# Kernel optimization log

Hardware: AMD Instinct MI355X
Metric: run time of the kernel (lower is better)

Reference implementation:

```python
import jax, jax.numpy as jnp
import numpy as np

D = 256      # model dim
H = 8        # heads
DH = 32      # dim per head
M = 110      # nb random features = int(32*ln(32))
DEPTH = 6
DFF = 1024   # ff_mult * D


def _layer_norm(x, g, b):
    mu = jnp.mean(x, -1, keepdims=True)
    var = jnp.mean(jnp.square(x - mu), -1, keepdims=True)
    return (x - mu) * jax.lax.rsqrt(var + 1e-5) * g + b


def _softmax_kernel(x, proj, is_query):
    # FAVOR+ positive softmax kernel features (performer-pytorch softmax_kernel)
    dn = x.shape[-1] ** -0.25
    ratio = proj.shape[0] ** -0.5
    xd = jnp.einsum('bhnd,md->bhnm', x * dn, proj)
    diag = 0.5 * jnp.sum(jnp.square(x), -1, keepdims=True) * dn * dn
    stab = jnp.max(xd, -1, keepdims=True) if is_query else jnp.max(xd)
    return ratio * (jnp.exp(xd - diag - stab) + 1e-3)


def _linear_attention(q, k, v):
    # non-causal linear attention: O(N*m*d) instead of O(N^2)
    k_sum = jnp.sum(k, axis=2)                               # [B,H,m]
    d_inv = 1.0 / jnp.einsum('bhnm,bhm->bhn', q, k_sum)      # [B,H,N]
    ctx = jnp.einsum('bhnm,bhnd->bhmd', k, v)                # [B,H,m,dh]
    return jnp.einsum('bhnm,bhmd,bhn->bhnd', q, ctx, d_inv)


def _forward(expr, token_emb, cls_token, ln1_g, ln1_b, Wq, bq, Wk, bk, Wv, bv,
             Wo, bo, ln2_g, ln2_b, W1, b1, W2, b2, proj_mat, Wp, bp, top_k_genes):
    B = expr.shape[0]
    vals, _ = jax.lax.top_k(expr, top_k_genes)               # [B, k] sorted desc (matches torch.topk)
    # preprocess: L1 normalize (eps=1e-12 like F.normalize) -> *1e4 -> log1p -> 7 bins
    norm = vals / jnp.maximum(jnp.sum(jnp.abs(vals), -1, keepdims=True), 1e-12)
    e = jnp.log1p(norm * 10000.0)
    bins = jnp.linspace(0.0, jnp.max(e), 8)
    # torch.bucketize(right=False) == searchsorted side='left'
    tokens = jnp.clip(jnp.searchsorted(bins[:-1], e, side='left'), 0, 6)
    x = jnp.concatenate([jnp.broadcast_to(cls_token, (B, 1, D)), token_emb[tokens]], axis=1)
    N = x.shape[1]
    for i in range(DEPTH):
        # pre-norm FAVOR+ attention block
        h = _layer_norm(x, ln1_g[i], ln1_b[i])
        q = (h @ Wq[i] + bq[i]).reshape(B, N, H, DH).transpose(0, 2, 1, 3)
        k = (h @ Wk[i] + bk[i]).reshape(B, N, H, DH).transpose(0, 2, 1, 3)
        v = (h @ Wv[i] + bv[i]).reshape(B, N, H, DH).transpose(0, 2, 1, 3)
        qp = _softmax_kernel(q, proj_mat[i], True)
        kp = _softmax_kernel(k, proj_mat[i], False)
        o = _linear_attention(qp, kp, v).transpose(0, 2, 1, 3).reshape(B, N, D)
        x = x + o @ Wo[i] + bo[i]
        # pre-norm FFN block (GELU exact, like torch default)
        h2 = _layer_norm(x, ln2_g[i], ln2_b[i])
        x = x + jax.nn.gelu(h2 @ W1[i] + b1[i], approximate=False) @ W2[i] + b2[i]
    return x[:, 0] @ Wp + bp


def setup_inputs() -> dict:
    key = jax.random.key(0)
    ks = jax.random.split(key, 12)
    s = 0.02
    return {
        'expr': jax.random.uniform(ks[0], (8, 16906), dtype=jnp.float32),
        'token_emb': jax.random.normal(ks[1], (7, D), dtype=jnp.float32) * s,
        'cls_token': jax.random.normal(ks[2], (1, 1, D), dtype=jnp.float32),
        'ln1_g': jnp.ones((DEPTH, D), jnp.float32),
        'ln1_b': jnp.zeros((DEPTH, D), jnp.float32),
        'Wq': jax.random.normal(ks[3], (DEPTH, D, D), dtype=jnp.float32) * s,
        'bq': jnp.zeros((DEPTH, D), jnp.float32),
        'Wk': jax.random.normal(ks[4], (DEPTH, D, D), dtype=jnp.float32) * s,
        'bk': jnp.zeros((DEPTH, D), jnp.float32),
        'Wv': jax.random.normal(ks[5], (DEPTH, D, D), dtype=jnp.float32) * s,
        'bv': jnp.zeros((DEPTH, D), jnp.float32),
        'Wo': jax.random.normal(ks[6], (DEPTH, D, D), dtype=jnp.float32) * s,
        'bo': jnp.zeros((DEPTH, D), jnp.float32),
        'ln2_g': jnp.ones((DEPTH, D), jnp.float32),
        'ln2_b': jnp.zeros((DEPTH, D), jnp.float32),
        'W1': jax.random.normal(ks[7], (DEPTH, D, DFF), dtype=jnp.float32) * s,
        'b1': jnp.zeros((DEPTH, DFF), jnp.float32),
        'W2': jax.random.normal(ks[8], (DEPTH, DFF, D), dtype=jnp.float32) * s,
        'b2': jnp.zeros((DEPTH, D), jnp.float32),
        'proj_mat': jax.random.normal(ks[9], (DEPTH, M, DH), dtype=jnp.float32),
        'Wp': jax.random.normal(ks[10], (D, D), dtype=jnp.float32) * s,
        'bp': jnp.zeros((D,), jnp.float32),
        'top_k_genes': 2048,
    }


def reference(expr, token_emb, cls_token, ln1_g, ln1_b, Wq, bq, Wk, bk, Wv, bv,
              Wo, bo, ln2_g, ln2_b, W1, b1, W2, b2, proj_mat, Wp, bp, top_k_genes):
    return _forward(expr, token_emb, cls_token, ln1_g, ln1_b, Wq, bq, Wk, bk, Wv, bv,
                    Wo, bo, ln2_g, ln2_b, W1, b1, W2, b2, proj_mat, Wp, bp, top_k_genes)
```

## Files before the change

kernel.cpp:

```cpp
#include <hip/hip_runtime.h>
#include <hip/hip_bf16.h>

#define B_    8
#define NG    16906
#define KSEL  2048
#define D_    256
#define H_    8
#define DH    32
#define M_    110
#define DEPTH_ 6
#define DFF_  1024
#define N_    2049
#define BN_   (B_*N_)
#define QS    768
#define NC    8
#define NTILES 33
#define CTXE  (M_*33)
#define CTXN2 (64*CTXE)
#define NIT_TK 17

static constexpr float DN    = 0.42044820762685725f;
static constexpr float DN2   = 0.17677669529663687f;
static constexpr float RATIO = 0.09534625892455922f;

typedef __attribute__((ext_vector_type(8))) short s8v;
typedef __attribute__((ext_vector_type(4))) float f4v;

__device__ __forceinline__ unsigned floatToOrdered(float f){
  unsigned b = __float_as_uint(f);
  return (b & 0x80000000u) ? ~b : (b | 0x80000000u);
}
__device__ __forceinline__ float orderedToFloat(unsigned u){
  unsigned b = (u & 0x80000000u) ? (u & 0x7FFFFFFFu) : ~u;
  return __uint_as_float(b);
}
__device__ __forceinline__ unsigned short f2us(float f){
  __hip_bfloat16 b = __float2bfloat16(f);
  return *reinterpret_cast<unsigned short*>(&b);
}

__global__ __launch_bounds__(1024) void topk_k(const float* __restrict__ expr,
                                               float* __restrict__ selected)
{
  __shared__ unsigned hist[256];
  __shared__ unsigned sPrefix;
  __shared__ int sKK;
  __shared__ unsigned cGT, cEQ;
  int b = blockIdx.x, tid = threadIdx.x;
  const float* row = expr + (long)b*NG;
  unsigned rb[NIT_TK];
  #pragma unroll
  for (int i = 0; i < NIT_TK; i++){
    int idx = tid + i*1024;
    rb[i] = (idx < NG) ? __float_as_uint(row[idx]) : 0u;
  }
  if (tid == 0){ sPrefix = 0u; sKK = KSEL; }
  __syncthreads();
  for (int pass = 0; pass < 4; ++pass){
    int shift = 24 - pass*8;
    if (tid < 256) hist[tid] = 0u;
    __syncthreads();
    unsigned pref = sPrefix;
    #pragma unroll
    for (int i = 0; i < NIT_TK; i++){
      int idx = tid + i*1024;
      unsigned bits = rb[i];
      bool ok = (idx < NG) && ((pass == 0) || ((bits >> (shift + 8)) == pref));
      if (ok) atomicAdd(&hist[(bits >> shift) & 255u], 1u);
    }
    __syncthreads();
    if (tid == 0){
      int kk = sKK; unsigned cum = 0; int sel = 0;
      for (int j = 255; j >= 0; --j){
        unsigned c = hist[j];
        if (cum + c >= (unsigned)kk){ sel = j; break; }
        cum += c;
      }
      sPrefix = (pref << 8) | (unsigned)sel;
      sKK = kk - (int)cum;
    }
    __syncthreads();
  }
  unsigned T = sPrefix; int needEQ = sKK; int base = KSEL - needEQ;
  if (tid == 0){ cGT = 0u; cEQ = 0u; }
  __syncthreads();
  #pragma unroll
  for (int i = 0; i < NIT_TK; i++){
    int idx = tid + i*1024;
    if (idx < NG){
      unsigned bits = rb[i];
      if (bits > T){
        unsigned p = atomicAdd(&cGT, 1u);
        selected[(long)b*KSEL + p] = __uint_as_float(bits);
      } else if (bits == T){
        unsigned p = atomicAdd(&cEQ, 1u);
        if ((int)p < needEQ) selected[(long)b*KSEL + base + p] = __uint_as_float(bits);
      }
    }
  }
}

__global__ __launch_bounds__(256) void nsum_k(const float* __restrict__ selected,
                                              float* __restrict__ bsum, float* __restrict__ bv0)
{
  __shared__ float rs[256], rm[256];
  int b = blockIdx.x, tid = threadIdx.x;
  float s = 0.f, m = -INFINITY;
  for (int i = tid; i < KSEL; i += 256){ float v = selected[(long)b*KSEL + i]; s += v; m = fmaxf(m, v); }
  rs[tid] = s; rm[tid] = m; __syncthreads();
  for (int k = 128; k > 0; k >>= 1){
    if (tid < k){ rs[tid] += rs[tid + k]; rm[tid] = fmaxf(rm[tid], rm[tid + k]); }
    __syncthreads();
  }
  if (tid == 0){ bsum[b] = rs[0]; bv0[b] = rm[0]; }
}

__global__ __launch_bounds__(64) void emax_k(const float* __restrict__ bsum,
                                             const float* __restrict__ bv0,
                                             float* __restrict__ emaxp)
{
  int tid = threadIdx.x;
  float e = -INFINITY;
  if (tid < B_) e = log1pf(bv0[tid] / fmaxf(bsum[tid], 1e-12f) * 10000.0f);
  #pragma unroll
  for (int m = 1; m < 64; m <<= 1) e = fmaxf(e, __shfl_xor(e, m));
  if (tid == 0) emaxp[0] = e;
}

__global__ __launch_bounds__(64) void embed_k(const float* __restrict__ selected,
    const float* __restrict__ bsum, const float* __restrict__ emaxp,
    const float* __restrict__ temb, const float* __restrict__ cls,
    float* __restrict__ x)
{
  int rowi = blockIdx.x;
  int b = rowi / N_, n = rowi % N_;
  int tid = threadIdx.x;
  const float* src;
  if (n == 0){
    src = cls;
  } else {
    float val = selected[(long)b*KSEL + (n - 1)];
    float e = log1pf(val / fmaxf(bsum[b], 1e-12f) * 10000.0f);
    float step = emaxp[0] / 7.0f;
    int cnt = 0;
    #pragma unroll
    for (int i = 0; i < 7; i++) cnt += (((float)i * step) < e) ? 1 : 0;
    int tok = cnt > 6 ? 6 : cnt;
    src = temb + (long)tok * D_;
  }
  float4 o = *(const float4*)(src + tid*4);
  *(float4*)(x + (long)rowi*D_ + tid*4) = o;
}

__global__ __launch_bounds__(256) void ln_k(const float* __restrict__ x,
    unsigned short* __restrict__ out,
    const float* __restrict__ g, const float* __restrict__ bb)
{
  int row = blockIdx.x*4 + (threadIdx.x >> 6);
  int lane = threadIdx.x & 63;
  float4 v = *(const float4*)(x + (long)row*D_ + lane*4);
  float s = v.x + v.y + v.z + v.w;
  float q = v.x*v.x + v.y*v.y + v.z*v.z + v.w*v.w;
  #pragma unroll
  for (int m = 1; m < 64; m <<= 1){ s += __shfl_xor(s, m); q += __shfl_xor(q, m); }
  float mu  = s * (1.0f/D_);
  float var = q * (1.0f/D_) - mu*mu;
  float inv = 1.0f / sqrtf(fmaxf(var, 0.f) + 1e-5f);
  float4 gu = *(const float4*)(g + lane*4);
  float4 bu = *(const float4*)(bb + lane*4);
  ushort4 o;
  o.x = f2us((v.x - mu)*inv*gu.x + bu.x);
  o.y = f2us((v.y - mu)*inv*gu.y + bu.y);
  o.z = f2us((v.z - mu)*inv*gu.z + bu.z);
  o.w = f2us((v.w - mu)*inv*gu.w + bu.w);
  *(ushort4*)(out + (long)row*D_ + lane*4) = o;
}

__global__ __launch_bounds__(256) void wcvt_k(const float* __restrict__ src, long srcL,
    unsigned short* __restrict__ dst, long dstL, int K, int N)
{
  __shared__ float t[32][33];
  int n0 = blockIdx.x*32, k0 = blockIdx.y*32, L = blockIdx.z;
  int tx = threadIdx.x & 31, ty = threadIdx.x >> 5;
  const float* s = src + (long)L*srcL;
  for (int i = ty; i < 32; i += 8)
    t[i][tx] = s[(long)(k0+i)*N + n0 + tx];
  __syncthreads();
  unsigned short* d = dst + (long)L*dstL;
  for (int i = ty; i < 32; i += 8)
    d[(long)(n0 + i)*K + k0 + tx] = f2us(t[tx][i]);
}

__global__ __launch_bounds__(256) void pcvt_k(const float* __restrict__ proj,
                                              unsigned short* __restrict__ projb,
                                              unsigned* __restrict__ kmaxb)
{
  int L = blockIdx.x;
  if (blockIdx.x == 0 && threadIdx.x < DEPTH_) kmaxb[threadIdx.x] = 0u;
  for (int i = threadIdx.x; i < 112*32; i += 256){
    int m = i >> 5, d = i & 31;
    float v = (m < M_) ? proj[(long)L*M_*DH + m*DH + d] : 0.f;
    projb[(long)L*112*32 + i] = f2us(v);
  }
}

__global__ __launch_bounds__(256) void bcat_k(const float* __restrict__ bq,
    const float* __restrict__ bk, const float* __restrict__ bv,
    float* __restrict__ bqkv)
{
  int L = blockIdx.x;
  for (int i = threadIdx.x; i < QS; i += 256){
    float v = (i < 256) ? bq[L*256 + i] : (i < 512) ? bk[L*256 + i - 256] : bv[L*256 + i - 512];
    bqkv[(long)L*QS + i] = v;
  }
}

template<int ACT, int RES, int OUTBF>
__global__ __launch_bounds__(256) void bgemm_k(
    const unsigned short* __restrict__ A, long lda,
    const unsigned short* __restrict__ Bt,
    const float* __restrict__ bias,
    const float* __restrict__ res,
    float* __restrict__ Cf, unsigned short* __restrict__ Cb,
    int M, int Nn, int K)
{
  __shared__ __attribute__((aligned(16))) unsigned short As[128*40];
  __shared__ __attribute__((aligned(16))) unsigned short Bs[128*40];
  int tid = threadIdx.x;
  int rowBlk = blockIdx.x*128, colBlk = blockIdx.y*128;
  int w = tid >> 6, lane = tid & 63;
  int wrow = (w >> 1)*64, wcol = (w & 1)*64;
  int fr = lane & 15, fk = (lane >> 4)*8, fq = lane >> 4;
  int srh = tid >> 2, sk8 = (tid & 3)*8;

  f4v acc[4][4];
  #pragma unroll
  for (int r = 0; r < 4; r++)
    #pragma unroll
    for (int c = 0; c < 4; c++) acc[r][c] = (f4v){0.f, 0.f, 0.f, 0.f};

  s8v pa[2], pb[2];
  #pragma unroll
  for (int half = 0; half < 2; half++){
    int r = half*64 + srh;
    int ar = rowBlk + r;
    pa[half] = (ar < M) ? *(const s8v*)(A + (long)ar*lda + sk8) : (s8v){0,0,0,0,0,0,0,0};
    pb[half] = *(const s8v*)(Bt + (long)(colBlk + r)*K + sk8);
  }

  for (int kt = 0; kt < K; kt += 32){
    __syncthreads();
    #pragma unroll
    for (int half = 0; half < 2; half++){
      int r = half*64 + srh;
      *(s8v*)&As[r*40 + sk8] = pa[half];
      *(s8v*)&Bs[r*40 + sk8] = pb[half];
    }
    __syncthreads();
    if (kt + 32 < K){
      int kn = kt + 32;
      #pragma unroll
      for (int half = 0; half < 2; half++){
        int r = half*64 + srh;
        int ar = rowBlk + r;
        pa[half] = (ar < M) ? *(const s8v*)(A + (long)ar*lda + kn + sk8) : (s8v){0,0,0,0,0,0,0,0};
        pb[half] = *(const s8v*)(Bt + (long)(colBlk + r)*K + kn + sk8);
      }
    }
    s8v a[4], b[4];
    #pragma unroll
    for (int r = 0; r < 4; r++) a[r] = *(s8v*)&As[(wrow + r*16 + fr)*40 + fk];
    #pragma unroll
    for (int c = 0; c < 4; c++) b[c] = *(s8v*)&Bs[(wcol + c*16 + fr)*40 + fk];
    #pragma unroll
    for (int r = 0; r < 4; r++)
      #pragma unroll
      for (int c = 0; c < 4; c++)
        acc[r][c] = __builtin_amdgcn_mfma_f32_16x16x32_bf16(a[r], b[c], acc[r][c], 0, 0, 0);
  }

  #pragma unroll
  for (int c = 0; c < 4; c++){
    int col = colBlk + wcol + c*16 + fr;
    float bz = bias[col];
    #pragma unroll
    for (int r = 0; r < 4; r++){
      #pragma unroll
      for (int j = 0; j < 4; j++){
        int row = rowBlk + wrow + r*16 + fq*4 + j;
        if (row < M){
          float val = acc[r][c][j] + bz;
          if (ACT == 1) val = 0.5f * val * (1.0f + erff(val * 0.70710678118654752f));
          if (RES) val += res[(long)row*Nn + col];
          if (OUTBF) Cb[(long)row*Nn + col] = f2us(val);
          else       Cf[(long)row*Nn + col] = val;
        }
      }
    }
  }
}

__global__ __launch_bounds__(256) void gemm_k(
    const float* __restrict__ A, long lda,
    const float* __restrict__ Bw, long ldb,
    const float* __restrict__ bias,
    float* __restrict__ Cf,
    int M, int Nn, int K)
{
  __shared__ float As[16][64];
  __shared__ float Bs[16][64];
  int tid = threadIdx.x;
  int tx = tid & 15, ty = tid >> 4;
  int rowBlk = blockIdx.x * 64, colBlk = blockIdx.y * 64;
  int am = tid >> 2, ak = (tid & 3) * 4;
  int bk = tid >> 4, bc = (tid & 15) * 4;
  float acc[4][4];
  #pragma unroll
  for (int i = 0; i < 4; i++)
    #pragma unroll
    for (int j = 0; j < 4; j++) acc[i][j] = 0.f;

  for (int kt = 0; kt < K; kt += 16){
    float4 av = make_float4(0.f, 0.f, 0.f, 0.f);
    int ar = rowBlk + am;
    if (ar < M) av = *(const float4*)(A + (long)ar*lda + kt + ak);
    As[ak+0][am] = av.x; As[ak+1][am] = av.y; As[ak+2][am] = av.z; As[ak+3][am] = av.w;
    float4 bv4 = *(const float4*)(Bw + (long)(kt + bk)*ldb + colBlk + bc);
    Bs[bk][bc+0] = bv4.x; Bs[bk][bc+1] = bv4.y;
    Bs[bk][bc+2] = bv4.z; Bs[bk][bc+3] = bv4.w;
    __syncthreads();
    #pragma unroll
    for (int kk = 0; kk < 16; kk++){
      float4 a4 = *(const float4*)&As[kk][ty*4];
      float4 b4 = *(const float4*)&Bs[kk][tx*4];
      acc[0][0] += a4.x*b4.x; acc[0][1] += a4.x*b4.y; acc[0][2] += a4.x*b4.z; acc[0][3] += a4.x*b4.w;
      acc[1][0] += a4.y*b4.x; acc[1][1] += a4.y*b4.y; acc[1][2] += a4.y*b4.z; acc[1][3] += a4.y*b4.w;
      acc[2][0] += a4.z*b4.x; acc[2][1] += a4.z*b4.y; acc[2][2] += a4.z*b4.z; acc[2][3] += a4.z*b4.w;
      acc[3][0] += a4.w*b4.x; acc[3][1] += a4.w*b4.y; acc[3][2] += a4.w*b4.z; acc[3][3] += a4.w*b4.w;
    }
    __syncthreads();
  }
  int r0 = rowBlk + ty*4, c0 = colBlk + tx*4;
  float bz[4];
  #pragma unroll
  for (int j = 0; j < 4; j++) bz[j] = bias[c0 + j];
  #pragma unroll
  for (int i = 0; i < 4; i++){
    int r = r0 + i;
    if (r < M){
      #pragma unroll
      for (int j = 0; j < 4; j++)
        Cf[(long)r*Nn + c0 + j] = acc[i][j] + bz[j];
    }
  }
}

__global__ __launch_bounds__(256) void kmax2_k(const float* __restrict__ qkv,
    const unsigned short* __restrict__ projb, unsigned* __restrict__ kmaxb)
{
  __shared__ __attribute__((aligned(16))) unsigned short ks[64*40];
  __shared__ float red[4];
  int t = blockIdx.x, h = blockIdx.y, b = blockIdx.z;
  int tid = threadIdx.x, w = tid >> 6, lane = tid & 63;
  int fr = lane & 15, fq = lane >> 4, fk = fq*8;
  int n0 = t*64;
  #pragma unroll
  for (int it = 0; it < 2; it++){
    int tok = it*32 + (tid >> 3), d4 = tid & 7;
    int n = n0 + tok;
    bool vld = (n < N_);
    long gb = ((long)(b*N_ + (vld ? n : 0)))*QS + 256 + h*DH + d4*4;
    float4 kv = vld ? *(const float4*)(qkv + gb) : make_float4(0,0,0,0);
    ushort4 ku; ku.x=f2us(kv.x); ku.y=f2us(kv.y); ku.z=f2us(kv.z); ku.w=f2us(kv.w);
    *(ushort4*)&ks[tok*40 + d4*4] = ku;
  }
  __syncthreads();
  s8v bk_ = *(s8v*)&ks[(w*16 + fr)*40 + fk];
  float mx = -INFINITY;
  int n_ = w*16 + fr;
  bool nv = (n0 + n_ < N_);
  #pragma unroll
  for (int mt = 0; mt < 7; mt++){
    s8v ap = *(const s8v*)(projb + (mt*16 + fr)*32 + fk);
    f4v z = (f4v){0.f,0.f,0.f,0.f};
    f4v xd = __builtin_amdgcn_mfma_f32_16x16x32_bf16(ap, bk_, z, 0, 0, 0);
    #pragma unroll
    for (int j = 0; j < 4; j++){
      int m = mt*16 + fq*4 + j;
      float v = (nv && m < M_) ? xd[j]*DN : -INFINITY;
      mx = fmaxf(mx, v);
    }
  }
  #pragma unroll
  for (int mk = 1; mk < 64; mk <<= 1) mx = fmaxf(mx, __shfl_xor(mx, mk));
  if (lane == 0) red[w] = mx;
  __syncthreads();
  if (tid == 0){
    float g = fmaxf(fmaxf(red[0], red[1]), fmaxf(red[2], red[3]));
    atomicMax(kmaxb, floatToOrdered(g));
  }
}

__global__ __launch_bounds__(256) void fctx_k(const float* __restrict__ qkv,
    const unsigned short* __restrict__ projb,
    const unsigned* __restrict__ kmaxb, float* __restrict__ partials)
{
  __shared__ __attribute__((aligned(16))) unsigned short ks[64*40];
  __shared__ __attribute__((aligned(16))) unsigned short vt[48*72];
  __shared__ __attribute__((aligned(16))) unsigned short kps[112*72];
  __shared__ float diags[64];
  int c = blockIdx.x, h = blockIdx.y, b = blockIdx.z;
  int tid = threadIdx.x, w = tid >> 6, lane = tid & 63;
  int fr = lane & 15, fq = lane >> 4, fk = fq*8;
  float kmax = orderedToFloat(kmaxb[0]);

  for (int i = tid; i < 15*72; i += 256) vt[33*72 + i] = 0;
  if (tid < 64) vt[32*72 + tid] = f2us(1.0f);

  s8v ap[7];
  #pragma unroll
  for (int mt = 0; mt < 7; mt++)
    ap[mt] = *(const s8v*)(projb + (mt*16 + fr)*32 + fk);

  int mt0 = w, mt1 = w + 4;
  f4v acc0[3], acc1[3];
  #pragma unroll
  for (int dt = 0; dt < 3; dt++){ acc0[dt] = (f4v){0.f,0.f,0.f,0.f}; acc1[dt] = (f4v){0.f,0.f,0.f,0.f}; }

  for (int t = c; t < NTILES; t += NC){
    int n0 = t*64;
    __syncthreads();
    #pragma unroll
    for (int it = 0; it < 2; it++){
      int tok = it*32 + (tid >> 3), d4 = tid & 7;
      int n = n0 + tok;
      bool vld = (n < N_);
      long gb = ((long)(b*N_ + (vld ? n : 0)))*QS + 256 + h*DH + d4*4;
      float4 kv = vld ? *(const float4*)(qkv + gb) : make_float4(0,0,0,0);
      float4 vv = vld ? *(const float4*)(qkv + gb + 256) : make_float4(0,0,0,0);
      ushort4 ku; ku.x=f2us(kv.x); ku.y=f2us(kv.y); ku.z=f2us(kv.z); ku.w=f2us(kv.w);
      *(ushort4*)&ks[tok*40 + d4*4] = ku;
      vt[(d4*4+0)*72 + tok] = f2us(vv.x);
      vt[(d4*4+1)*72 + tok] = f2us(vv.y);
      vt[(d4*4+2)*72 + tok] = f2us(vv.z);
      vt[(d4*4+3)*72 + tok] = f2us(vv.w);
      float sq = kv.x*kv.x + kv.y*kv.y + kv.z*kv.z + kv.w*kv.w;
      sq += __shfl_xor(sq, 1); sq += __shfl_xor(sq, 2); sq += __shfl_xor(sq, 4);
      if (d4 == 0) diags[tok] = 0.5f * DN2 * sq;
    }
    __syncthreads();
    s8v bk_ = *(s8v*)&ks[(w*16 + fr)*40 + fk];
    int n_ = w*16 + fr;
    bool nv = (n0 + n_ < N_);
    float dgn = diags[n_];
    #pragma unroll
    for (int mt = 0; mt < 7; mt++){
      f4v z = (f4v){0.f,0.f,0.f,0.f};
      f4v xd = __builtin_amdgcn_mfma_f32_16x16x32_bf16(ap[mt], bk_, z, 0, 0, 0);
      #pragma unroll
      for (int j = 0; j < 4; j++){
        float kp = nv ? RATIO*(expf(xd[j]*DN - dgn - kmax) + 1e-3f) : 0.f;
        kps[(mt*16 + fq*4 + j)*72 + n_] = f2us(kp);
      }
    }
    __syncthreads();
    #pragma unroll
    for (int kst = 0; kst < 2; kst++){
      int ko = kst*32 + fk;
      s8v b0 = *(s8v*)&vt[( 0 + fr)*72 + ko];
      s8v b1 = *(s8v*)&vt[(16 + fr)*72 + ko];
      s8v b2 = *(s8v*)&vt[(32 + fr)*72 + ko];
      s8v a0 = *(s8v*)&kps[(mt0*16 + fr)*72 + ko];
      acc0[0] = __builtin_amdgcn_mfma_f32_16x16x32_bf16(a0, b0, acc0[0], 0, 0, 0);
      acc0[1] = __builtin_amdgcn_mfma_f32_16x16x32_bf16(a0, b1, acc0[1], 0, 0, 0);
      acc0[2] = __builtin_amdgcn_mfma_f32_16x16x32_bf16(a0, b2, acc0[2], 0, 0, 0);
      if (mt1 < 7){
        s8v a1 = *(s8v*)&kps[(mt1*16 + fr)*72 + ko];
        acc1[0] = __builtin_amdgcn_mfma_f32_16x16x32_bf16(a1, b0, acc1[0], 0, 0, 0);
        acc1[1] = __builtin_amdgcn_mfma_f32_16x16x32_bf16(a1, b1, acc1[1], 0, 0, 0);
        acc1[2] = __builtin_amdgcn_mfma_f32_16x16x32_bf16(a1, b2, acc1[2], 0, 0, 0);
      }
    }
  }
  long pb = ((long)c*64 + (b*H_ + h))*CTXE;
  #pragma unroll
  for (int dt = 0; dt < 3; dt++){
    int d = dt*16 + fr;
    if (d < 33){
      #pragma unroll
      for (int j = 0; j < 4; j++){
        int m0 = mt0*16 + fq*4 + j;
        if (m0 < M_) partials[pb + m0*33 + d] = acc0[dt][j];
        if (mt1 < 7){
          int m1 = mt1*16 + fq*4 + j;
          if (m1 < M_) partials[pb + m1*33 + d] = acc1[dt][j];
        }
      }
    }
  }
}

__global__ __launch_bounds__(256) void ctxred2_k(const float* __restrict__ partials,
                                                 float* __restrict__ ctxf)
{
  int i = blockIdx.x*256 + threadIdx.x;
  if (i >= CTXN2) return;
  float s = 0.f;
  #pragma unroll
  for (int c = 0; c < NC; c++) s += partials[(long)c*CTXN2 + i];
  ctxf[i] = s;
}

__global__ __launch_bounds__(256) void attn3_k(const float* __restrict__ qkv,
    const float* __restrict__ ctxf, const unsigned short* __restrict__ projb,
    unsigned short* __restrict__ ob)
{
  __shared__ __attribute__((aligned(16))) unsigned short qs[64*40];
  __shared__ __attribute__((aligned(16))) unsigned short qps[64*136];
  __shared__ __attribute__((aligned(16))) unsigned short cst[48*136];
  __shared__ float diags[64];
  __shared__ float dens[64];
  int t = blockIdx.x, h = blockIdx.y, b = blockIdx.z;
  int tid = threadIdx.x, w = tid >> 6, lane = tid & 63;
  int fr = lane & 15, fq = lane >> 4, fk = fq*8;
  int n0 = t*64;
  long cbase = ((long)(b*H_ + h))*CTXE;

  for (int i = tid; i < 64*16; i += 256)
    qps[(i >> 4)*136 + 112 + (i & 15)] = 0;

  #pragma unroll
  for (int it = 0; it < 2; it++){
    int tok = it*32 + (tid >> 3), d4 = tid & 7;
    int n = n0 + tok;
    bool vld = (n < N_);
    long gb = ((long)(b*N_ + (vld ? n : 0)))*QS + h*DH + d4*4;
    float4 qv = vld ? *(const float4*)(qkv + gb) : make_float4(0,0,0,0);
    ushort4 qu; qu.x=f2us(qv.x); qu.y=f2us(qv.y); qu.z=f2us(qv.z); qu.w=f2us(qv.w);
    *(ushort4*)&qs[tok*40 + d4*4] = qu;
    float sq = qv.x*qv.x + qv.y*qv.y + qv.z*qv.z + qv.w*qv.w;
    sq += __shfl_xor(sq, 1); sq += __shfl_xor(sq, 2); sq += __shfl_xor(sq, 4);
    if (d4 == 0) diags[tok] = 0.5f * DN2 * sq;
  }
  for (int i = tid; i < 48*128; i += 256){
    int d = i >> 7, m = i & 127;
    float v = (d < 33 && m < M_) ? ctxf[cbase + (long)m*33 + d] : 0.f;
    cst[d*136 + m] = f2us(v);
  }
  __syncthreads();

  s8v bq_ = *(s8v*)&qs[(w*16 + fr)*40 + fk];
  int n_ = w*16 + fr;
  bool nv = (n0 + n_ < N_);
  float dgn = diags[n_];
  f4v xdv[7];
  #pragma unroll
  for (int mt = 0; mt < 7; mt++){
    s8v ap = *(const s8v*)(projb + (mt*16 + fr)*32 + fk);
    f4v z = (f4v){0.f,0.f,0.f,0.f};
    xdv[mt] = __builtin_amdgcn_mfma_f32_16x16x32_bf16(ap, bq_, z, 0, 0, 0);
  }
  float mx = -INFINITY;
  #pragma unroll
  for (int mt = 0; mt < 7; mt++)
    #pragma unroll
    for (int j = 0; j < 4; j++){
      int m = mt*16 + fq*4 + j;
      if (m < M_) mx = fmaxf(mx, xdv[mt][j]*DN);
    }
  mx = fmaxf(mx, __shfl_xor(mx, 16));
  mx = fmaxf(mx, __shfl_xor(mx, 32));
  #pragma unroll
  for (int mt = 0; mt < 7; mt++)
    #pragma unroll
    for (int j = 0; j < 4; j++){
      int m = mt*16 + fq*4 + j;
      float qp = (nv && m < M_) ? RATIO*(expf(xdv[mt][j]*DN - dgn - mx) + 1e-3f) : 0.f;
      qps[n_*136 + m] = f2us(qp);
    }
  __syncthreads();

  f4v acc[3];
  acc[0] = (f4v){0,0,0,0}; acc[1] = (f4v){0,0,0,0}; acc[2] = (f4v){0,0,0,0};
  #pragma unroll
  for (int ks = 0; ks < 4; ks++){
    int ko = ks*32 + fk;
    s8v bqp = *(s8v*)&qps[(w*16 + fr)*136 + ko];
    #pragma unroll
    for (int dt = 0; dt < 3; dt++){
      s8v ac = *(s8v*)&cst[(dt*16 + fr)*136 + ko];
      acc[dt] = __builtin_amdgcn_mfma_f32_16x16x32_bf16(ac, bqp, acc[dt], 0, 0, 0);
    }
  }
  if (fq == 0) dens[n_] = acc[2][0];
  __syncthreads();
  float dinv = 1.0f / dens[n_];
  if (nv){
    long obase = ((long)(b*N_ + n0 + n_))*D_ + h*DH;
    #pragma unroll
    for (int dt = 0; dt < 2; dt++){
      ushort4 wv;
      wv.x = f2us(acc[dt][0]*dinv);
      wv.y = f2us(acc[dt][1]*dinv);
      wv.z = f2us(acc[dt][2]*dinv);
      wv.w = f2us(acc[dt][3]*dinv);
      *(ushort4*)(ob + obase + dt*16 + fq*4) = wv;
    }
  }
}

extern "C" void kernel_launch(void* const* d_in, const int* in_sizes, int n_in,
                              void* d_out, int out_size, void* d_ws, size_t ws_size,
                              hipStream_t stream)
{
  const float* expr = (const float*)d_in[0];
  const float* temb = (const float*)d_in[1];
  const float* cls  = (const float*)d_in[2];
  const float* ln1g = (const float*)d_in[3];
  const float* ln1b = (const float*)d_in[4];
  const float* Wq   = (const float*)d_in[5];
  const float* bq   = (const float*)d_in[6];
  const float* Wk   = (const float*)d_in[7];
  const float* bk   = (const float*)d_in[8];
  const float* Wv   = (const float*)d_in[9];
  const float* bv   = (const float*)d_in[10];
  const float* Wo   = (const float*)d_in[11];
  const float* bo   = (const float*)d_in[12];
  const float* ln2g = (const float*)d_in[13];
  const float* ln2b = (const float*)d_in[14];
  const float* W1   = (const float*)d_in[15];
  const float* b1   = (const float*)d_in[16];
  const float* W2   = (const float*)d_in[17];
  const float* b2   = (const float*)d_in[18];
  const float* proj = (const float*)d_in[19];
  const float* Wp   = (const float*)d_in[20];
  const float* bp   = (const float*)d_in[21];
  (void)in_sizes; (void)n_in; (void)out_size; (void)ws_size;

  char* w = (char*)d_ws;
  size_t off = 0;
  auto alloc = [&](size_t bytes) -> char* {
    char* p = w + off;
    off = (off + bytes + 255) & ~(size_t)255;
    return p;
  };
  float*    selected = (float*)alloc((size_t)B_*KSEL*4);
  float*    bsum     = (float*)alloc(B_*4);
  float*    bv0      = (float*)alloc(B_*4);
  float*    emaxp    = (float*)alloc(4);
  unsigned* kmaxb    = (unsigned*)alloc(DEPTH_*4);
  float*    ctxf     = (float*)alloc((size_t)CTXN2*4);
  float*          x  = (float*)alloc((size_t)BN_*D_*4);
  unsigned short* h  = (unsigned short*)alloc((size_t)BN_*D_*2);
  float*        qkv  = (float*)alloc((size_t)BN_*QS*4);
  unsigned short* Wqkvt = (unsigned short*)alloc((size_t)DEPTH_*QS*D_*2);
  unsigned short* Wot = (unsigned short*)alloc((size_t)DEPTH_*D_*D_*2);
  unsigned short* W1t = (unsigned short*)alloc((size_t)DEPTH_*D_*DFF_*2);
  unsigned short* W2t = (unsigned short*)alloc((size_t)DEPTH_*DFF_*D_*2);
  unsigned short* projb = (unsigned short*)alloc((size_t)DEPTH_*112*32*2);
  float*    bqkv     = (float*)alloc((size_t)DEPTH_*QS*4);
  unsigned short* ffi = (unsigned short*)qkv;
  float*     partials = (float*)h;

  wcvt_k<<<dim3(8, 8, DEPTH_),  256, 0, stream>>>(Wq, (long)D_*D_, Wqkvt + 0,      (long)QS*D_, D_, D_);
  wcvt_k<<<dim3(8, 8, DEPTH_),  256, 0, stream>>>(Wk, (long)D_*D_, Wqkvt + 256*D_, (long)QS*D_, D_, D_);
  wcvt_k<<<dim3(8, 8, DEPTH_),  256, 0, stream>>>(Wv, (long)D_*D_, Wqkvt + 512*D_, (long)QS*D_, D_, D_);
  wcvt_k<<<dim3(8, 8, DEPTH_),  256, 0, stream>>>(Wo, (long)D_*D_,   Wot, (long)D_*D_,   D_, D_);
  wcvt_k<<<dim3(32, 8, DEPTH_), 256, 0, stream>>>(W1, (long)D_*DFF_, W1t, (long)D_*DFF_, D_, DFF_);
  wcvt_k<<<dim3(8, 32, DEPTH_), 256, 0, stream>>>(W2, (long)DFF_*D_, W2t, (long)DFF_*D_, DFF_, D_);
  pcvt_k<<<DEPTH_, 256, 0, stream>>>(proj, projb, kmaxb);
  bcat_k<<<DEPTH_, 256, 0, stream>>>(bq, bk, bv, bqkv);

  topk_k<<<B_, 1024, 0, stream>>>(expr, selected);
  nsum_k<<<B_, 256, 0, stream>>>(selected, bsum, bv0);
  emax_k<<<1, 64, 0, stream>>>(bsum, bv0, emaxp);
  embed_k<<<BN_, 64, 0, stream>>>(selected, bsum, emaxp, temb, cls, x);

  for (int L = 0; L < DEPTH_; L++){
    const unsigned short* pjb = projb + (size_t)L*112*32;
    ln_k<<<BN_/4, 256, 0, stream>>>(x, h, ln1g + L*D_, ln1b + L*D_);
    bgemm_k<0,0,0><<<dim3(129,6), 256, 0, stream>>>(h, D_, Wqkvt + (size_t)L*QS*D_, bqkv + (size_t)L*QS, nullptr, qkv, nullptr, BN_, QS, D_);
    kmax2_k<<<dim3(NTILES, H_, B_), 256, 0, stream>>>(qkv, pjb, kmaxb + L);
    fctx_k<<<dim3(NC, H_, B_), 256, 0, stream>>>(qkv, pjb, kmaxb + L, partials);
    ctxred2_k<<<(CTXN2 + 255)/256, 256, 0, stream>>>(partials, ctxf);
    attn3_k<<<dim3(NTILES, H_, B_), 256, 0, stream>>>(qkv, ctxf, pjb, h);
    bgemm_k<0,1,0><<<dim3(129,2), 256, 0, stream>>>(h, D_, Wot + (size_t)L*D_*D_, bo + L*D_, x, x, nullptr, BN_, D_, D_);
    ln_k<<<BN_/4, 256, 0, stream>>>(x, h, ln2g + L*D_, ln2b + L*D_);
    bgemm_k<1,0,1><<<dim3(129,8), 256, 0, stream>>>(h, D_, W1t + (size_t)L*D_*DFF_, b1 + L*DFF_, nullptr, nullptr, ffi, BN_, DFF_, D_);
    bgemm_k<0,1,0><<<dim3(129,2), 256, 0, stream>>>(ffi, DFF_, W2t + (size_t)L*DFF_*D_, b2 + L*D_, x, x, nullptr, BN_, D_, DFF_);
  }
  gemm_k<<<dim3(1,4), 256, 0, stream>>>(x, (long)N_*D_, Wp, D_, bp,
                                        (float*)d_out, B_, D_, D_);
}
```

Before: 1.539 ms.

## Privatize topk histograms, aggregate atomics, stage bf16 GEMM output, swap grid order

The top-k radix select now uses one histogram per wavefront to reduce atomic contention, and it does the final scatter with wave-level ballot aggregation instead of per-thread atomics. The bf16-output GEMM epilogue (the FFN up-projection with GELU) writes its tile to shared memory first and then stores it with coalesced 16-byte writes. GEMM grids are transposed so that column blocks vary fastest, meant to improve reuse of A rows across consecutive blocks. The staging buffer enlarges shared memory for the OUTBF variant, which may reduce occupancy.

Measured after the change: 1.426 ms. 1.08x faster.

```diff
diff --git a/kernel.cpp b/kernel.cpp
--- a/kernel.cpp
+++ b/kernel.cpp
@@ -42,11 +42,12 @@
 __global__ __launch_bounds__(1024) void topk_k(const float* __restrict__ expr,
                                                float* __restrict__ selected)
 {
-  __shared__ unsigned hist[256];
+  __shared__ unsigned histw[16*256];
   __shared__ unsigned sPrefix;
   __shared__ int sKK;
   __shared__ unsigned cGT, cEQ;
   int b = blockIdx.x, tid = threadIdx.x;
+  int wv = tid >> 6, lane = tid & 63;
   const float* row = expr + (long)b*NG;
   unsigned rb[NIT_TK];
   #pragma unroll
@@ -55,10 +56,9 @@
     rb[i] = (idx < NG) ? __float_as_uint(row[idx]) : 0u;
   }
   if (tid == 0){ sPrefix = 0u; sKK = KSEL; }
-  __syncthreads();
   for (int pass = 0; pass < 4; ++pass){
     int shift = 24 - pass*8;
-    if (tid < 256) hist[tid] = 0u;
+    for (int i = tid; i < 16*256; i += 1024) histw[i] = 0u;
     __syncthreads();
     unsigned pref = sPrefix;
     #pragma unroll
@@ -66,13 +66,20 @@
       int idx = tid + i*1024;
       unsigned bits = rb[i];
       bool ok = (idx < NG) && ((pass == 0) || ((bits >> (shift + 8)) == pref));
-      if (ok) atomicAdd(&hist[(bits >> shift) & 255u], 1u);
+      if (ok) atomicAdd(&histw[wv*256 + ((bits >> shift) & 255u)], 1u);
+    }
+    __syncthreads();
+    if (tid < 256){
+      unsigned s = 0;
+      #pragma unroll
+      for (int w = 0; w < 16; w++) s += histw[w*256 + tid];
+      histw[tid] = s;
     }
     __syncthreads();
     if (tid == 0){
       int kk = sKK; unsigned cum = 0; int sel = 0;
       for (int j = 255; j >= 0; --j){
-        unsigned c = hist[j];
+        unsigned c = histw[j];
         if (cum + c >= (unsigned)kk){ sel = j; break; }
         cum += c;
       }
@@ -87,14 +94,30 @@
   #pragma unroll
   for (int i = 0; i < NIT_TK; i++){
     int idx = tid + i*1024;
-    if (idx < NG){
-      unsigned bits = rb[i];
-      if (bits > T){
-        unsigned p = atomicAdd(&cGT, 1u);
-        selected[(long)b*KSEL + p] = __uint_as_float(bits);
-      } else if (bits == T){
-        unsigned p = atomicAdd(&cEQ, 1u);
-        if ((int)p < needEQ) selected[(long)b*KSEL + base + p] = __uint_as_float(bits);
+    bool v = (idx < NG);
+    unsigned bits = rb[i];
+    bool gt = v && (bits > T);
+    unsigned long long mgt = __ballot(gt);
+    if (mgt){
+      int leader = __ffsll((long long)mgt) - 1;
+      unsigned wbase = 0;
+      if (lane == leader) wbase = atomicAdd(&cGT, (unsigned)__popcll(mgt));
+      wbase = __shfl(wbase, leader);
+      if (gt){
+        int pre = __popcll(mgt & ((1ULL << lane) - 1ULL));
+        selected[(long)b*KSEL + wbase + pre] = __uint_as_float(bits);
+      }
+    }
+    bool eq = v && (bits == T);
+    unsigned long long meq = __ballot(eq);
+    if (meq){
+      int leader = __ffsll((long long)meq) - 1;
+      unsigned wbase = 0;
+      if (lane == leader) wbase = atomicAdd(&cEQ, (unsigned)__popcll(meq));
+      wbase = __shfl(wbase, leader);
+      if (eq){
+        int pos = (int)wbase + __popcll(meq & ((1ULL << lane) - 1ULL));
+        if (pos < needEQ) selected[(long)b*KSEL + base + pos] = __uint_as_float(bits);
       }
     }
   }
@@ -224,10 +247,11 @@
     float* __restrict__ Cf, unsigned short* __restrict__ Cb,
     int M, int Nn, int K)
 {
-  __shared__ __attribute__((aligned(16))) unsigned short As[128*40];
-  __shared__ __attribute__((aligned(16))) unsigned short Bs[128*40];
+  __shared__ __attribute__((aligned(16))) unsigned short smem[OUTBF ? 128*132 : 2*128*40];
+  unsigned short* As = smem;
+  unsigned short* Bs = smem + 128*40;
   int tid = threadIdx.x;
-  int rowBlk = blockIdx.x*128, colBlk = blockIdx.y*128;
+  int colBlk = blockIdx.x*128, rowBlk = blockIdx.y*128;
   int w = tid >> 6, lane = tid & 63;
   int wrow = (w >> 1)*64, wcol = (w & 1)*64;
   int fr = lane & 15, fk = (lane >> 4)*8, fq = lane >> 4;
@@ -279,21 +303,47 @@
         acc[r][c] = __builtin_amdgcn_mfma_f32_16x16x32_bf16(a[r], b[c], acc[r][c], 0, 0, 0);
   }
 
-  #pragma unroll
-  for (int c = 0; c < 4; c++){
-    int col = colBlk + wcol + c*16 + fr;
-    float bz = bias[col];
-    #pragma unroll
-    for (int r = 0; r < 4; r++){
+  if (OUTBF){
+    __syncthreads();
+    unsigned short* Cs = smem;
+    #pragma unroll
+    for (int c = 0; c < 4; c++){
+      int col = wcol + c*16 + fr;
+      float bz = bias[colBlk + col];
       #pragma unroll
-      for (int j = 0; j < 4; j++){
-        int row = rowBlk + wrow + r*16 + fq*4 + j;
-        if (row < M){
+      for (int r = 0; r < 4; r++){
+        #pragma unroll
+        for (int j = 0; j < 4; j++){
+          int rrow = wrow + r*16 + fq*4 + j;
           float val = acc[r][c][j] + bz;
           if (ACT == 1) val = 0.5f * val * (1.0f + erff(val * 0.70710678118654752f));
-          if (RES) val += res[(long)row*Nn + col];
-          if (OUTBF) Cb[(long)row*Nn + col] = f2us(val);
-          else       Cf[(long)row*Nn + col] = val;
+          Cs[rrow*132 + col] = f2us(val);
+        }
+      }
+    }
+    __syncthreads();
+    for (int ci = tid; ci < 128*16; ci += 256){
+      int rrow = ci >> 4, ch = ci & 15;
+      int grow = rowBlk + rrow;
+      if (grow < M)
+        *(s8v*)(Cb + (long)grow*Nn + colBlk + ch*8) = *(s8v*)&Cs[rrow*132 + ch*8];
+    }
+  } else {
+    #pragma unroll
+    for (int c = 0; c < 4; c++){
+      int col = colBlk + wcol + c*16 + fr;
+      float bz = bias[col];
+      #pragma unroll
+      for (int r = 0; r < 4; r++){
+        #pragma unroll
+        for (int j = 0; j < 4; j++){
+          int row = rowBlk + wrow + r*16 + fq*4 + j;
+          if (row < M){
+            float val = acc[r][c][j] + bz;
+            if (ACT == 1) val = 0.5f * val * (1.0f + erff(val * 0.70710678118654752f));
+            if (RES) val += res[(long)row*Nn + col];
+            Cf[(long)row*Nn + col] = val;
+          }
         }
       }
     }
@@ -679,15 +729,15 @@
   for (int L = 0; L < DEPTH_; L++){
     const unsigned short* pjb = projb + (size_t)L*112*32;
     ln_k<<<BN_/4, 256, 0, stream>>>(x, h, ln1g + L*D_, ln1b + L*D_);
-    bgemm_k<0,0,0><<<dim3(129,6), 256, 0, stream>>>(h, D_, Wqkvt + (size_t)L*QS*D_, bqkv + (size_t)L*QS, nullptr, qkv, nullptr, BN_, QS, D_);
+    bgemm_k<0,0,0><<<dim3(6,129), 256, 0, stream>>>(h, D_, Wqkvt + (size_t)L*QS*D_, bqkv + (size_t)L*QS, nullptr, qkv, nullptr, BN_, QS, D_);
     kmax2_k<<<dim3(NTILES, H_, B_), 256, 0, stream>>>(qkv, pjb, kmaxb + L);
     fctx_k<<<dim3(NC, H_, B_), 256, 0, stream>>>(qkv, pjb, kmaxb + L, partials);
     ctxred2_k<<<(CTXN2 + 255)/256, 256, 0, stream>>>(partials, ctxf);
     attn3_k<<<dim3(NTILES, H_, B_), 256, 0, stream>>>(qkv, ctxf, pjb, h);
-    bgemm_k<0,1,0><<<dim3(129,2), 256, 0, stream>>>(h, D_, Wot + (size_t)L*D_*D_, bo + L*D_, x, x, nullptr, BN_, D_, D_);
+    bgemm_k<0,1,0><<<dim3(2,129), 256, 0, stream>>>(h, D_, Wot + (size_t)L*D_*D_, bo + L*D_, x, x, nullptr, BN_, D_, D_);
     ln_k<<<BN_/4, 256, 0, stream>>>(x, h, ln2g + L*D_, ln2b + L*D_);
-    bgemm_k<1,0,1><<<dim3(129,8), 256, 0, stream>>>(h, D_, W1t + (size_t)L*D_*DFF_, b1 + L*DFF_, nullptr, nullptr, ffi, BN_, DFF_, D_);
-    bgemm_k<0,1,0><<<dim3(129,2), 256, 0, stream>>>(ffi, DFF_, W2t + (size_t)L*DFF_*D_, b2 + L*D_, x, x, nullptr, BN_, D_, DFF_);
+    bgemm_k<1,0,1><<<dim3(8,129), 256, 0, stream>>>(h, D_, W1t + (size_t)L*D_*DFF_, b1 + L*DFF_, nullptr, nullptr, ffi, BN_, DFF_, D_);
+    bgemm_k<0,1,0><<<dim3(2,129), 256, 0, stream>>>(ffi, DFF_, W2t + (size_t)L*DFF_*D_, b2 + L*D_, x, x, nullptr, BN_, D_, DFF_);
   }
   gemm_k<<<dim3(1,4), 256, 0, stream>>>(x, (long)N_*D_, Wp, D_, bp,
                                         (float*)d_out, B_, D_, D_);
```
